# Optimization experiments

Hardware: AMD Instinct MI355X
Metric: run time of the kernel (lower is better)

Reference implementation:

```python
import jax, jax.numpy as jnp
import numpy as np

NUM_NODES = 100000
EMB = 16
LAT = 8
EDGE_DIM = 32
E = 1600000


def setup_inputs() -> dict:
    key = jax.random.key(0)
    ks = jax.random.split(key, 12)
    s = 0.05
    return {
        "edge_index": jax.random.randint(ks[0], (2, E), 0, NUM_NODES),
        "edge_attr": jax.random.normal(ks[1], (E, EDGE_DIM), dtype=jnp.float32),
        "node_emb": jax.random.normal(ks[2], (NUM_NODES, EMB), dtype=jnp.float32) * s,
        "ew_W1": jax.random.normal(ks[3], (EDGE_DIM, 64), dtype=jnp.float32) * s,
        "ew_b1": jnp.zeros((64,), jnp.float32),
        "ew_W2": jax.random.normal(ks[4], (64, EMB * LAT), dtype=jnp.float32) * s,
        "ew_b2": jnp.zeros((EMB * LAT,), jnp.float32),
        "root_W": jax.random.normal(ks[5], (EMB, LAT), dtype=jnp.float32) * s,
        "conv_b": jnp.zeros((LAT,), jnp.float32),
        "dec_W1": jax.random.normal(ks[6], (2 * LAT, 64), dtype=jnp.float32) * s,
        "dec_b1": jnp.zeros((64,), jnp.float32),
        "dec_W2": jax.random.normal(ks[7], (64, EDGE_DIM), dtype=jnp.float32) * s,
        "dec_b2": jnp.zeros((EDGE_DIM,), jnp.float32),
    }


def reference(edge_index, edge_attr, node_emb, ew_W1, ew_b1, ew_W2, ew_b2,
              root_W, conv_b, dec_W1, dec_b1, dec_W2, dec_b2):
    src, tgt = edge_index[0], edge_index[1]
    # edge MLP -> per-edge weight matrix (E, EMB, LAT)
    h = jax.nn.relu(edge_attr @ ew_W1 + ew_b1)
    theta = (h @ ew_W2 + ew_b2).reshape(-1, EMB, LAT)
    # per-edge matmul on gathered source features
    msg = jnp.einsum('ei,eio->eo', node_emb[src], theta)  # (E, LAT)
    # scatter-mean to targets
    agg = jax.ops.segment_sum(msg, tgt, num_segments=NUM_NODES)
    cnt = jax.ops.segment_sum(jnp.ones((msg.shape[0],), msg.dtype), tgt, num_segments=NUM_NODES)
    agg = agg / jnp.maximum(cnt, 1.0)[:, None]
    # NNConv root weight + bias
    latent = node_emb @ root_W + agg + conv_b  # (N, LAT)
    # decode: gather-concat-MLP on edges
    edge_in = jnp.concatenate([latent[src], latent[tgt]], axis=1)  # (E, 2*LAT)
    out = jax.nn.relu(edge_in @ dec_W1 + dec_b1) @ dec_W2 + dec_b2  # (E, EDGE_DIM)
    return out
```

## Files before the change

### kernel.cpp

```cpp
#include <hip/hip_runtime.h>
#include <hip/hip_bf16.h>

typedef __attribute__((ext_vector_type(8))) short  s16x8;
typedef __attribute__((ext_vector_type(4))) float  f32x4;

constexpr int EMB  = 16;
constexpr int LAT  = 8;
constexpr int EDIM = 32;
constexpr int HID  = 64;

constexpr int BSHIFT = 7;
constexpr int BNODES = 1 << BSHIFT;
constexpr int PCHUNK = 8192;

__device__ __forceinline__ short f2b(float f) {
  __hip_bfloat16 h = __float2bfloat16(f);
  return __builtin_bit_cast(short, h);
}
__device__ __forceinline__ float asf(unsigned int u) { return __builtin_bit_cast(float, u); }
__device__ __forceinline__ unsigned int pk2(float lo, float hi) {
  return ((unsigned int)(unsigned short)f2b(hi) << 16) |
         (unsigned int)(unsigned short)f2b(lo);
}

#define FIXSCALE 1.0995116277760e12f
#define FIXINV   9.094947017729282e-13

__global__ void prep_kernel(const float* __restrict__ W1, const float* __restrict__ W2,
                            const float* __restrict__ b2,
                            const float* __restrict__ dW1, const float* __restrict__ dW2,
                            short* __restrict__ W1c, short* __restrict__ W2p,
                            unsigned int* __restrict__ b2pp,
                            short* __restrict__ dW1c, short* __restrict__ dW2p) {
  int t = blockIdx.x * blockDim.x + threadIdx.x;
  if (t < 64 * 32) { int c = t / 32, k = t % 32; W1c[t] = f2b(W1[k * 64 + c]); }
  if (t < 8192) {
    int ct2 = t >> 10, kt = (t >> 9) & 1, lh = (t >> 7) & 3, r = (t >> 3) & 15, j = t & 7;
    int k = (kt * 2 + (j >> 2)) * 16 + lh * 4 + (j & 3);
    int i = 2 * ct2 + ((r >> 1) & 1);
    int o = 2 * (r >> 2) + (r & 1);
    W2p[t] = f2b(W2[k * 128 + i * 8 + o]);
  }
  if (t < 64) {
    int lh = t >> 4, slot = t & 15;
    int ct2 = slot >> 1, ih = slot & 1;
    int i = 2 * ct2 + ih;
    unsigned int lo = (unsigned short)f2b(b2[i * 8 + 2 * lh]);
    unsigned int hi = (unsigned short)f2b(b2[i * 8 + 2 * lh + 1]);
    b2pp[t] = (hi << 16) | lo;
  }
  if (t < 64 * 16) { int c = t / 16, k = t % 16; dW1c[t] = f2b(dW1[k * 64 + c]); }
  if (t < 2048) {
    int ct2 = t >> 10, kt = (t >> 9) & 1, lh = (t >> 7) & 3, r = (t >> 3) & 15, j = t & 7;
    int k = (kt * 2 + (j >> 2)) * 16 + lh * 4 + (j & 3);
    dW2p[t] = f2b(dW2[k * 32 + ct2 * 16 + r]);
  }
}

__global__ __launch_bounds__(256) void bhist_kernel(const int* __restrict__ ei,
                                                    int* __restrict__ bins,
                                                    int E, int nbuck) {
  __shared__ int h[1024];
  for (int i = threadIdx.x; i < nbuck; i += 256) h[i] = 0;
  __syncthreads();
  for (int e = blockIdx.x * blockDim.x + threadIdx.x; e < E; e += gridDim.x * blockDim.x)
    atomicAdd(&h[ei[E + e] >> BSHIFT], 1);
  __syncthreads();
  for (int i = threadIdx.x; i < nbuck; i += 256)
    if (h[i]) atomicAdd(&bins[i], h[i]);
}

__global__ __launch_bounds__(1024) void bscan_kernel(const int* __restrict__ bins,
                                                     int* __restrict__ bases,
                                                     int* __restrict__ cursor, int nbuck) {
  __shared__ int sh[1024];
  int tid = threadIdx.x;
  int v = (tid < nbuck) ? bins[tid] : 0;
  sh[tid] = v;
  __syncthreads();
  for (int off = 1; off < 1024; off <<= 1) {
    int t = (tid >= off) ? sh[tid - off] : 0;
    __syncthreads();
    sh[tid] += t;
    __syncthreads();
  }
  int ex = sh[tid] - v;
  if (tid < nbuck) { bases[tid] = ex; cursor[tid] = ex; }
  if (tid == 0) bases[nbuck] = sh[1023];
}

__global__ __launch_bounds__(256) void part_kernel(const int* __restrict__ ei,
                                                   int* __restrict__ cursor,
                                                   unsigned int* __restrict__ recs,
                                                   int E, int nbuck) {
  __shared__ int h[1024];
  __shared__ int gcl[1024];
  __shared__ int lr[1024];
  const int tid  = threadIdx.x;
  const int base = blockIdx.x * PCHUNK;

  for (int i = tid; i < nbuck; i += 256) { h[i] = 0; lr[i] = 0; }
  __syncthreads();
  for (int i = tid; i < PCHUNK; i += 256) {
    int e = base + i;
    if (e < E) atomicAdd(&h[ei[E + e] >> BSHIFT], 1);
  }
  __syncthreads();
  for (int i = tid; i < nbuck; i += 256)
    gcl[i] = h[i] ? atomicAdd(&cursor[i], h[i]) : 0;
  __syncthreads();
  for (int i = tid; i < PCHUNK; i += 256) {
    int e = base + i;
    if (e >= E) continue;
    int tgt = ei[E + e];
    int b = tgt >> BSHIFT;
    int p = gcl[b] + atomicAdd(&lr[b], 1);
    recs[p] = ((unsigned int)e << BSHIFT) | (unsigned int)(tgt & (BNODES - 1));
  }
}

__global__ __launch_bounds__(256, 3) void enc_mfma_kernel(
    const int* __restrict__ ei, const float* __restrict__ attr,
    const float* __restrict__ emb,
    const short* __restrict__ W1c, const float* __restrict__ b1,
    const short* __restrict__ W2p, const unsigned int* __restrict__ b2pp,
    short* __restrict__ ms, int E) {
  __shared__ short lds_w1[2048];
  __shared__ short lds_w2[8192];
  __shared__ float lds_b1[64];
  __shared__ unsigned int lds_b2[64];

  const int tid = threadIdx.x;
  const int w = tid >> 6, l = tid & 63;
  const int lh = l >> 4, ll = l & 15;
  const int ebase = blockIdx.x * 256 + w * 64;

  {
    reinterpret_cast<int4*>(lds_w1)[tid] = reinterpret_cast<const int4*>(W1c)[tid];
#pragma unroll
    for (int i = 0; i < 4; i++)
      reinterpret_cast<int4*>(lds_w2)[i * 256 + tid] =
          reinterpret_cast<const int4*>(W2p)[i * 256 + tid];
    if (tid < 64) lds_b1[tid] = b1[tid];
    if (tid < 64) lds_b2[tid] = b2pp[tid];
  }

  unsigned int xqp[8];
  {
    int ec = min(ebase + l, E - 1);
    int src = ei[ec];
    const float4* er = reinterpret_cast<const float4*>(emb) + (size_t)src * 4;
    float4 v0 = er[0], v1 = er[1], v2 = er[2], v3 = er[3];
    xqp[0] = pk2(v0.x, v0.y); xqp[1] = pk2(v0.z, v0.w);
    xqp[2] = pk2(v1.x, v1.y); xqp[3] = pk2(v1.z, v1.w);
    xqp[4] = pk2(v2.x, v2.y); xqp[5] = pk2(v2.z, v2.w);
    xqp[6] = pk2(v3.x, v3.y); xqp[7] = pk2(v3.z, v3.w);
  }

  s16x8 afs[4];
#pragma unroll
  for (int mt = 0; mt < 4; mt++) {
    int rowA = min(ebase + mt * 16 + ll, E - 1);
    const float4* ap = reinterpret_cast<const float4*>(attr + (size_t)rowA * EDIM + lh * 8);
    float4 a0 = ap[0], a1 = ap[1];
    afs[mt][0]=f2b(a0.x); afs[mt][1]=f2b(a0.y); afs[mt][2]=f2b(a0.z); afs[mt][3]=f2b(a0.w);
    afs[mt][4]=f2b(a1.x); afs[mt][5]=f2b(a1.y); afs[mt][6]=f2b(a1.z); afs[mt][7]=f2b(a1.w);
  }

  __syncthreads();

  const f32x4 z = {0.f, 0.f, 0.f, 0.f};

#pragma unroll
  for (int mt = 0; mt < 4; mt++) {
    f32x4 c1t[4];
#pragma unroll
    for (int ct = 0; ct < 4; ct++) {
      s16x8 b1f = *reinterpret_cast<const s16x8*>(lds_w1 + (ct * 16 + ll) * 32 + lh * 8);
      c1t[ct] = __builtin_amdgcn_mfma_f32_16x16x32_bf16(b1f, afs[mt], z, 0, 0, 0);
    }

    short hb[4][4];
#pragma unroll
    for (int ct = 0; ct < 4; ct++) {
      float4 bv = *reinterpret_cast<const float4*>(lds_b1 + ct * 16 + lh * 4);
      hb[ct][0] = f2b(fmaxf(c1t[ct][0] + bv.x, 0.f));
      hb[ct][1] = f2b(fmaxf(c1t[ct][1] + bv.y, 0.f));
      hb[ct][2] = f2b(fmaxf(c1t[ct][2] + bv.z, 0.f));
      hb[ct][3] = f2b(fmaxf(c1t[ct][3] + bv.w, 0.f));
    }
    s16x8 a2f0, a2f1;
#pragma unroll
    for (int j = 0; j < 8; j++) a2f0[j] = hb[(j >> 2)][j & 3];
#pragma unroll
    for (int j = 0; j < 8; j++) a2f1[j] = hb[2 + (j >> 2)][j & 3];

    const int srcl = mt * 16 + ll;
    unsigned int xs[8];
#pragma unroll
    for (int c = 0; c < 8; c++)
      xs[c] = (unsigned int)__shfl((int)xqp[c], srcl, 64);

    float q0 = 0.f, q1 = 0.f;
#pragma unroll
    for (int ct2 = 0; ct2 < 8; ct2++) {
      s16x8 f0 = *reinterpret_cast<const s16x8*>(lds_w2 + ((ct2 * 2 + 0) * 4 + lh) * 128 + ll * 8);
      s16x8 f1 = *reinterpret_cast<const s16x8*>(lds_w2 + ((ct2 * 2 + 1) * 4 + lh) * 128 + ll * 8);
      f32x4 c2 = __builtin_amdgcn_mfma_f32_16x16x32_bf16(f0, a2f0, z, 0, 0, 0);
      c2 = __builtin_amdgcn_mfma_f32_16x16x32_bf16(f1, a2f1, c2, 0, 0, 0);
      uint2 pp = *reinterpret_cast<const uint2*>(lds_b2 + lh * 16 + 2 * ct2);
      float b00 = asf(pp.x << 16), b01 = asf(pp.x & 0xffff0000u);
      float b10 = asf(pp.y << 16), b11 = asf(pp.y & 0xffff0000u);
      float xv0 = asf(xs[ct2] << 16);
      float xv1 = asf(xs[ct2] & 0xffff0000u);
      q0 = fmaf(xv0, c2[0] + b00, q0);
      q1 = fmaf(xv0, c2[1] + b01, q1);
      q0 = fmaf(xv1, c2[2] + b10, q0);
      q1 = fmaf(xv1, c2[3] + b11, q1);
    }
    int e = ebase + mt * 16 + ll;
    if (e < E)
      *reinterpret_cast<unsigned int*>(ms + (size_t)e * LAT + 2 * lh) = pk2(q0, q1);
  }
}

__global__ __launch_bounds__(256) void agg_kernel(
    const float* __restrict__ emb, const short* __restrict__ ms,
    const unsigned int* __restrict__ recs, const int* __restrict__ bases,
    const float* __restrict__ rootW, const float* __restrict__ convb,
    float* __restrict__ latent, int N) {
  __shared__ long long acc[BNODES][LAT];
  __shared__ int cnt[BNODES];
  __shared__ float rw[EMB * LAT];
  __shared__ float cb[LAT];

  const int tid = threadIdx.x;
  const int b = blockIdx.x;

  long long* af = &acc[0][0];
  for (int i = tid; i < BNODES * LAT; i += 256) af[i] = 0;
  if (tid < BNODES) cnt[tid] = 0;
  if (tid < EMB * LAT) rw[tid] = rootW[tid];
  if (tid < LAT) cb[tid] = convb[tid];
  __syncthreads();

  const int s = bases[b], epos = bases[b + 1];
  const uint4* mp = reinterpret_cast<const uint4*>(ms);
  for (int i = s + tid; i < epos; i += 256) {
    unsigned int r = recs[i];
    int eid = (int)(r >> BSHIFT);
    int tl  = (int)(r & (BNODES - 1));
    uint4 m = mp[(size_t)eid];
    float f0 = asf(m.x << 16), f1 = asf(m.x & 0xffff0000u);
    float f2 = asf(m.y << 16), f3 = asf(m.y & 0xffff0000u);
    float f4 = asf(m.z << 16), f5 = asf(m.z & 0xffff0000u);
    float f6 = asf(m.w << 16), f7 = asf(m.w & 0xffff0000u);
    atomicAdd((unsigned long long*)&acc[tl][0], (unsigned long long)(long long)(f0 * FIXSCALE));
    atomicAdd((unsigned long long*)&acc[tl][1], (unsigned long long)(long long)(f1 * FIXSCALE));
    atomicAdd((unsigned long long*)&acc[tl][2], (unsigned long long)(long long)(f2 * FIXSCALE));
    atomicAdd((unsigned long long*)&acc[tl][3], (unsigned long long)(long long)(f3 * FIXSCALE));
    atomicAdd((unsigned long long*)&acc[tl][4], (unsigned long long)(long long)(f4 * FIXSCALE));
    atomicAdd((unsigned long long*)&acc[tl][5], (unsigned long long)(long long)(f5 * FIXSCALE));
    atomicAdd((unsigned long long*)&acc[tl][6], (unsigned long long)(long long)(f6 * FIXSCALE));
    atomicAdd((unsigned long long*)&acc[tl][7], (unsigned long long)(long long)(f7 * FIXSCALE));
    atomicAdd(&cnt[tl], 1);
  }
  __syncthreads();

  int n = b * BNODES + tid;
  if (tid < BNODES && n < N) {
    float inv = 1.f / fmaxf((float)cnt[tid], 1.f);
    float r[LAT];
#pragma unroll
    for (int o = 0; o < LAT; o++)
      r[o] = fmaf((float)((double)acc[tid][o] * FIXINV), inv, cb[o]);

    float x[EMB];
    const float4* np4 = reinterpret_cast<const float4*>(emb) + (size_t)n * (EMB / 4);
#pragma unroll
    for (int i = 0; i < EMB / 4; i++) {
      float4 v = np4[i];
      x[4 * i + 0] = v.x; x[4 * i + 1] = v.y; x[4 * i + 2] = v.z; x[4 * i + 3] = v.w;
    }
#pragma unroll
    for (int i = 0; i < EMB; i++)
#pragma unroll
      for (int o = 0; o < LAT; o++) r[o] = fmaf(x[i], rw[i * LAT + o], r[o]);

    float4* lp = reinterpret_cast<float4*>(latent) + (size_t)n * 2;
    lp[0] = make_float4(r[0], r[1], r[2], r[3]);
    lp[1] = make_float4(r[4], r[5], r[6], r[7]);
  }
}

__global__ __launch_bounds__(256, 4) void dec_mfma_kernel(
    const int* __restrict__ ei, const float* __restrict__ lat,
    const short* __restrict__ dW1c, const float* __restrict__ db1,
    const short* __restrict__ dW2p, const float* __restrict__ db2,
    float* __restrict__ out, int E) {
  __shared__ short lds_w1[2048];
  __shared__ short lds_w2[2048];
  __shared__ float lds_b1[64];
  __shared__ float lds_b2[32];

  const int tid = threadIdx.x;
  const int w = tid >> 6, l = tid & 63;
  const int lh = l >> 4, ll = l & 15;
  const int ebase = blockIdx.x * 256 + w * 64;

  {
    if (tid < 128) {
      int4 v = reinterpret_cast<const int4*>(dW1c)[tid];
      int hid = tid >> 1, kb = (tid & 1) * 8;
      *reinterpret_cast<int4*>(lds_w1 + hid * 32 + kb) = v;
      *reinterpret_cast<int4*>(lds_w1 + hid * 32 + 16 + kb) = make_int4(0, 0, 0, 0);
    }
    reinterpret_cast<int4*>(lds_w2)[tid] = reinterpret_cast<const int4*>(dW2p)[tid];
    if (tid < 64) lds_b1[tid] = db1[tid];
    if (tid < 32) lds_b2[tid] = db2[tid];
  }
  __syncthreads();

  const f32x4 z = {0.f, 0.f, 0.f, 0.f};

#pragma unroll
  for (int mt = 0; mt < 4; mt++) {
    s16x8 af = (s16x8){0, 0, 0, 0, 0, 0, 0, 0};
    if (lh < 2) {
      int rowA = min(ebase + mt * 16 + ll, E - 1);
      int node = ei[(lh == 0 ? 0 : E) + rowA];
      const float4* lp = reinterpret_cast<const float4*>(lat + (size_t)node * LAT);
      float4 p0 = lp[0], p1 = lp[1];
      af[0]=f2b(p0.x); af[1]=f2b(p0.y); af[2]=f2b(p0.z); af[3]=f2b(p0.w);
      af[4]=f2b(p1.x); af[5]=f2b(p1.y); af[6]=f2b(p1.z); af[7]=f2b(p1.w);
    }

    f32x4 c1t[4];
#pragma unroll
    for (int ct = 0; ct < 4; ct++) {
      s16x8 b1f = *reinterpret_cast<const s16x8*>(lds_w1 + (ct * 16 + ll) * 32 + lh * 8);
      c1t[ct] = __builtin_amdgcn_mfma_f32_16x16x32_bf16(b1f, af, z, 0, 0, 0);
    }

    short hb[4][4];
#pragma unroll
    for (int ct = 0; ct < 4; ct++) {
      float4 bv = *reinterpret_cast<const float4*>(lds_b1 + ct * 16 + lh * 4);
      hb[ct][0] = f2b(fmaxf(c1t[ct][0] + bv.x, 0.f));
      hb[ct][1] = f2b(fmaxf(c1t[ct][1] + bv.y, 0.f));
      hb[ct][2] = f2b(fmaxf(c1t[ct][2] + bv.z, 0.f));
      hb[ct][3] = f2b(fmaxf(c1t[ct][3] + bv.w, 0.f));
    }
    s16x8 a2f0, a2f1;
#pragma unroll
    for (int j = 0; j < 8; j++) a2f0[j] = hb[(j >> 2)][j & 3];
#pragma unroll
    for (int j = 0; j < 8; j++) a2f1[j] = hb[2 + (j >> 2)][j & 3];

    int e = ebase + mt * 16 + ll;
#pragma unroll
    for (int ct2 = 0; ct2 < 2; ct2++) {
      s16x8 f0 = *reinterpret_cast<const s16x8*>(lds_w2 + ((ct2 * 2 + 0) * 4 + lh) * 128 + ll * 8);
      s16x8 f1 = *reinterpret_cast<const s16x8*>(lds_w2 + ((ct2 * 2 + 1) * 4 + lh) * 128 + ll * 8);
      f32x4 c2 = __builtin_amdgcn_mfma_f32_16x16x32_bf16(f0, a2f0, z, 0, 0, 0);
      c2 = __builtin_amdgcn_mfma_f32_16x16x32_bf16(f1, a2f1, c2, 0, 0, 0);
      float4 bv = *reinterpret_cast<const float4*>(lds_b2 + ct2 * 16 + lh * 4);
      if (e < E)
        *reinterpret_cast<float4*>(out + (size_t)e * EDIM + ct2 * 16 + lh * 4) =
            make_float4(c2[0] + bv.x, c2[1] + bv.y, c2[2] + bv.z, c2[3] + bv.w);
    }
  }
}

extern "C" void kernel_launch(void* const* d_in, const int* in_sizes, int n_in,
                              void* d_out, int out_size, void* d_ws, size_t ws_size,
                              hipStream_t stream) {
  const int*   ei    = (const int*)  d_in[0];
  const float* attr  = (const float*)d_in[1];
  const float* emb   = (const float*)d_in[2];
  const float* ewW1  = (const float*)d_in[3];
  const float* ewb1  = (const float*)d_in[4];
  const float* ewW2  = (const float*)d_in[5];
  const float* ewb2  = (const float*)d_in[6];
  const float* rootW = (const float*)d_in[7];
  const float* convb = (const float*)d_in[8];
  const float* dW1   = (const float*)d_in[9];
  const float* db1   = (const float*)d_in[10];
  const float* dW2   = (const float*)d_in[11];
  const float* db2   = (const float*)d_in[12];
  float* out = (float*)d_out;

  const int E     = in_sizes[0] / 2;
  const int N     = in_sizes[2] / EMB;
  const int nbuck = (N + BNODES - 1) >> BSHIFT;

  short* W1c  = (short*)d_ws;
  short* W2p  = W1c + 64 * 32;
  short* dW1c = W2p + 8192;
  short* dW2p = dW1c + 64 * 16;
  unsigned int* b2pp = (unsigned int*)(dW2p + 2048);
  short* ms   = (short*)(b2pp + 64);
  float* lat  = (float*)(ms + (size_t)E * LAT);
  unsigned int* recs = (unsigned int*)(lat + (size_t)N * LAT);
  int* bins   = (int*)(recs + E);
  int* bases  = bins + nbuck;
  int* cursor = bases + nbuck + 1;

  const int blocks_e = (E + 255) / 256;
  const int blocks_p = (E + PCHUNK - 1) / PCHUNK;

  hipMemsetAsync(bins, 0, (size_t)nbuck * sizeof(int), stream);
  prep_kernel<<<32, 256, 0, stream>>>(ewW1, ewW2, ewb2, dW1, dW2,
                                      W1c, W2p, b2pp, dW1c, dW2p);
  bhist_kernel<<<256, 256, 0, stream>>>(ei, bins, E, nbuck);
  bscan_kernel<<<1, 1024, 0, stream>>>(bins, bases, cursor, nbuck);
  part_kernel<<<blocks_p, 256, 0, stream>>>(ei, cursor, recs, E, nbuck);
  enc_mfma_kernel<<<blocks_e, 256, 0, stream>>>(ei, attr, emb, W1c, ewb1, W2p, b2pp,
                                                ms, E);
  agg_kernel<<<nbuck, 256, 0, stream>>>(emb, ms, recs, bases, rootW, convb, lat, N);
  dec_mfma_kernel<<<blocks_e, 256, 0, stream>>>(ei, lat, dW1c, db1, dW2p, db2, out, E);
}
```

Baseline: 220.7 us.

## Fuse edge encoder into bucketed aggregation kernel, dropping per-edge message buffer

Merges the per-edge MLP/message kernel into the target-bucket aggregation kernel. Each block walks its bucket's sorted edge records, computes messages with MFMA and accumulates them straight into LDS fixed-point accumulators, so the intermediate message array is never written to or read back from global memory. In exchange, edge_attr and source embeddings are now read in target-sorted, scattered order rather than coalesced, occupancy drops from three to two blocks per CU, and per-block work follows the uneven bucket sizes with only 782 blocks.

```diff
diff --git a/kernel.cpp b/kernel.cpp
--- a/kernel.cpp
+++ b/kernel.cpp
@@ -119,21 +119,27 @@
   }
 }
 
-__global__ __launch_bounds__(256, 3) void enc_mfma_kernel(
+__global__ __launch_bounds__(256, 2) void encagg_kernel(
     const int* __restrict__ ei, const float* __restrict__ attr,
     const float* __restrict__ emb,
     const short* __restrict__ W1c, const float* __restrict__ b1,
     const short* __restrict__ W2p, const unsigned int* __restrict__ b2pp,
-    short* __restrict__ ms, int E) {
+    const unsigned int* __restrict__ recs, const int* __restrict__ bases,
+    const float* __restrict__ rootW, const float* __restrict__ convb,
+    float* __restrict__ latent, int N, int E) {
   __shared__ short lds_w1[2048];
   __shared__ short lds_w2[8192];
   __shared__ float lds_b1[64];
   __shared__ unsigned int lds_b2[64];
+  __shared__ long long acc[BNODES][LAT];
+  __shared__ int cnt[BNODES];
+  __shared__ float rw[EMB * LAT];
+  __shared__ float cb[LAT];
 
   const int tid = threadIdx.x;
   const int w = tid >> 6, l = tid & 63;
   const int lh = l >> 4, ll = l & 15;
-  const int ebase = blockIdx.x * 256 + w * 64;
+  const int b = blockIdx.x;
 
   {
     reinterpret_cast<int4*>(lds_w1)[tid] = reinterpret_cast<const int4*>(W1c)[tid];
@@ -143,127 +149,99 @@
           reinterpret_cast<const int4*>(W2p)[i * 256 + tid];
     if (tid < 64) lds_b1[tid] = b1[tid];
     if (tid < 64) lds_b2[tid] = b2pp[tid];
-  }
-
-  unsigned int xqp[8];
-  {
-    int ec = min(ebase + l, E - 1);
-    int src = ei[ec];
-    const float4* er = reinterpret_cast<const float4*>(emb) + (size_t)src * 4;
-    float4 v0 = er[0], v1 = er[1], v2 = er[2], v3 = er[3];
-    xqp[0] = pk2(v0.x, v0.y); xqp[1] = pk2(v0.z, v0.w);
-    xqp[2] = pk2(v1.x, v1.y); xqp[3] = pk2(v1.z, v1.w);
-    xqp[4] = pk2(v2.x, v2.y); xqp[5] = pk2(v2.z, v2.w);
-    xqp[6] = pk2(v3.x, v3.y); xqp[7] = pk2(v3.z, v3.w);
-  }
-
-  s16x8 afs[4];
-#pragma unroll
-  for (int mt = 0; mt < 4; mt++) {
-    int rowA = min(ebase + mt * 16 + ll, E - 1);
-    const float4* ap = reinterpret_cast<const float4*>(attr + (size_t)rowA * EDIM + lh * 8);
-    float4 a0 = ap[0], a1 = ap[1];
-    afs[mt][0]=f2b(a0.x); afs[mt][1]=f2b(a0.y); afs[mt][2]=f2b(a0.z); afs[mt][3]=f2b(a0.w);
-    afs[mt][4]=f2b(a1.x); afs[mt][5]=f2b(a1.y); afs[mt][6]=f2b(a1.z); afs[mt][7]=f2b(a1.w);
-  }
-
-  __syncthreads();
-
+    long long* af0 = &acc[0][0];
+    for (int i = tid; i < BNODES * LAT; i += 256) af0[i] = 0;
+    if (tid < BNODES) cnt[tid] = 0;
+    if (tid < EMB * LAT) rw[tid] = rootW[tid];
+    if (tid < LAT) cb[tid] = convb[tid];
+  }
+  __syncthreads();
+
+  const int s = bases[b], epos = bases[b + 1];
+  const int nrec = epos - s;
   const f32x4 z = {0.f, 0.f, 0.f, 0.f};
 
-#pragma unroll
-  for (int mt = 0; mt < 4; mt++) {
-    f32x4 c1t[4];
-#pragma unroll
-    for (int ct = 0; ct < 4; ct++) {
-      s16x8 b1f = *reinterpret_cast<const s16x8*>(lds_w1 + (ct * 16 + ll) * 32 + lh * 8);
-      c1t[ct] = __builtin_amdgcn_mfma_f32_16x16x32_bf16(b1f, afs[mt], z, 0, 0, 0);
-    }
-
-    short hb[4][4];
-#pragma unroll
-    for (int ct = 0; ct < 4; ct++) {
-      float4 bv = *reinterpret_cast<const float4*>(lds_b1 + ct * 16 + lh * 4);
-      hb[ct][0] = f2b(fmaxf(c1t[ct][0] + bv.x, 0.f));
-      hb[ct][1] = f2b(fmaxf(c1t[ct][1] + bv.y, 0.f));
-      hb[ct][2] = f2b(fmaxf(c1t[ct][2] + bv.z, 0.f));
-      hb[ct][3] = f2b(fmaxf(c1t[ct][3] + bv.w, 0.f));
-    }
-    s16x8 a2f0, a2f1;
-#pragma unroll
-    for (int j = 0; j < 8; j++) a2f0[j] = hb[(j >> 2)][j & 3];
-#pragma unroll
-    for (int j = 0; j < 8; j++) a2f1[j] = hb[2 + (j >> 2)][j & 3];
-
-    const int srcl = mt * 16 + ll;
-    unsigned int xs[8];
-#pragma unroll
-    for (int c = 0; c < 8; c++)
-      xs[c] = (unsigned int)__shfl((int)xqp[c], srcl, 64);
-
-    float q0 = 0.f, q1 = 0.f;
-#pragma unroll
-    for (int ct2 = 0; ct2 < 8; ct2++) {
-      s16x8 f0 = *reinterpret_cast<const s16x8*>(lds_w2 + ((ct2 * 2 + 0) * 4 + lh) * 128 + ll * 8);
-      s16x8 f1 = *reinterpret_cast<const s16x8*>(lds_w2 + ((ct2 * 2 + 1) * 4 + lh) * 128 + ll * 8);
-      f32x4 c2 = __builtin_amdgcn_mfma_f32_16x16x32_bf16(f0, a2f0, z, 0, 0, 0);
-      c2 = __builtin_amdgcn_mfma_f32_16x16x32_bf16(f1, a2f1, c2, 0, 0, 0);
-      uint2 pp = *reinterpret_cast<const uint2*>(lds_b2 + lh * 16 + 2 * ct2);
-      float b00 = asf(pp.x << 16), b01 = asf(pp.x & 0xffff0000u);
-      float b10 = asf(pp.y << 16), b11 = asf(pp.y & 0xffff0000u);
-      float xv0 = asf(xs[ct2] << 16);
-      float xv1 = asf(xs[ct2] & 0xffff0000u);
-      q0 = fmaf(xv0, c2[0] + b00, q0);
-      q1 = fmaf(xv0, c2[1] + b01, q1);
-      q0 = fmaf(xv1, c2[2] + b10, q0);
-      q1 = fmaf(xv1, c2[3] + b11, q1);
-    }
-    int e = ebase + mt * 16 + ll;
-    if (e < E)
-      *reinterpret_cast<unsigned int*>(ms + (size_t)e * LAT + 2 * lh) = pk2(q0, q1);
-  }
-}
-
-__global__ __launch_bounds__(256) void agg_kernel(
-    const float* __restrict__ emb, const short* __restrict__ ms,
-    const unsigned int* __restrict__ recs, const int* __restrict__ bases,
-    const float* __restrict__ rootW, const float* __restrict__ convb,
-    float* __restrict__ latent, int N) {
-  __shared__ long long acc[BNODES][LAT];
-  __shared__ int cnt[BNODES];
-  __shared__ float rw[EMB * LAT];
-  __shared__ float cb[LAT];
-
-  const int tid = threadIdx.x;
-  const int b = blockIdx.x;
-
-  long long* af = &acc[0][0];
-  for (int i = tid; i < BNODES * LAT; i += 256) af[i] = 0;
-  if (tid < BNODES) cnt[tid] = 0;
-  if (tid < EMB * LAT) rw[tid] = rootW[tid];
-  if (tid < LAT) cb[tid] = convb[tid];
-  __syncthreads();
-
-  const int s = bases[b], epos = bases[b + 1];
-  const uint4* mp = reinterpret_cast<const uint4*>(ms);
-  for (int i = s + tid; i < epos; i += 256) {
-    unsigned int r = recs[i];
-    int eid = (int)(r >> BSHIFT);
-    int tl  = (int)(r & (BNODES - 1));
-    uint4 m = mp[(size_t)eid];
-    float f0 = asf(m.x << 16), f1 = asf(m.x & 0xffff0000u);
-    float f2 = asf(m.y << 16), f3 = asf(m.y & 0xffff0000u);
-    float f4 = asf(m.z << 16), f5 = asf(m.z & 0xffff0000u);
-    float f6 = asf(m.w << 16), f7 = asf(m.w & 0xffff0000u);
-    atomicAdd((unsigned long long*)&acc[tl][0], (unsigned long long)(long long)(f0 * FIXSCALE));
-    atomicAdd((unsigned long long*)&acc[tl][1], (unsigned long long)(long long)(f1 * FIXSCALE));
-    atomicAdd((unsigned long long*)&acc[tl][2], (unsigned long long)(long long)(f2 * FIXSCALE));
-    atomicAdd((unsigned long long*)&acc[tl][3], (unsigned long long)(long long)(f3 * FIXSCALE));
-    atomicAdd((unsigned long long*)&acc[tl][4], (unsigned long long)(long long)(f4 * FIXSCALE));
-    atomicAdd((unsigned long long*)&acc[tl][5], (unsigned long long)(long long)(f5 * FIXSCALE));
-    atomicAdd((unsigned long long*)&acc[tl][6], (unsigned long long)(long long)(f6 * FIXSCALE));
-    atomicAdd((unsigned long long*)&acc[tl][7], (unsigned long long)(long long)(f7 * FIXSCALE));
-    atomicAdd(&cnt[tl], 1);
+  for (int g = w * 64; g < nrec; g += 256) {
+    const int base = s + g;
+    int ridx = min(base + l, epos - 1);
+    unsigned int rec = recs[ridx];
+    int eid = (int)(rec >> BSHIFT);
+    int tl  = (int)(rec & (BNODES - 1));
+    unsigned int xqp[8];
+    {
+      int src = ei[eid];
+      const float4* er = reinterpret_cast<const float4*>(emb) + (size_t)src * 4;
+      float4 v0 = er[0], v1 = er[1], v2 = er[2], v3 = er[3];
+      xqp[0] = pk2(v0.x, v0.y); xqp[1] = pk2(v0.z, v0.w);
+      xqp[2] = pk2(v1.x, v1.y); xqp[3] = pk2(v1.z, v1.w);
+      xqp[4] = pk2(v2.x, v2.y); xqp[5] = pk2(v2.z, v2.w);
+      xqp[6] = pk2(v3.x, v3.y); xqp[7] = pk2(v3.z, v3.w);
+    }
+    s16x8 afs[4];
+#pragma unroll
+    for (int mt = 0; mt < 4; mt++) {
+      int rowE = __shfl(eid, mt * 16 + ll, 64);
+      const float4* ap = reinterpret_cast<const float4*>(attr + (size_t)rowE * EDIM + lh * 8);
+      float4 a0 = ap[0], a1 = ap[1];
+      afs[mt][0]=f2b(a0.x); afs[mt][1]=f2b(a0.y); afs[mt][2]=f2b(a0.z); afs[mt][3]=f2b(a0.w);
+      afs[mt][4]=f2b(a1.x); afs[mt][5]=f2b(a1.y); afs[mt][6]=f2b(a1.z); afs[mt][7]=f2b(a1.w);
+    }
+
+#pragma unroll
+    for (int mt = 0; mt < 4; mt++) {
+      f32x4 c1t[4];
+#pragma unroll
+      for (int ct = 0; ct < 4; ct++) {
+        s16x8 b1f = *reinterpret_cast<const s16x8*>(lds_w1 + (ct * 16 + ll) * 32 + lh * 8);
+        c1t[ct] = __builtin_amdgcn_mfma_f32_16x16x32_bf16(b1f, afs[mt], z, 0, 0, 0);
+      }
+      short hb[4][4];
+#pragma unroll
+      for (int ct = 0; ct < 4; ct++) {
+        float4 bv = *reinterpret_cast<const float4*>(lds_b1 + ct * 16 + lh * 4);
+        hb[ct][0] = f2b(fmaxf(c1t[ct][0] + bv.x, 0.f));
+        hb[ct][1] = f2b(fmaxf(c1t[ct][1] + bv.y, 0.f));
+        hb[ct][2] = f2b(fmaxf(c1t[ct][2] + bv.z, 0.f));
+        hb[ct][3] = f2b(fmaxf(c1t[ct][3] + bv.w, 0.f));
+      }
+      s16x8 a2f0, a2f1;
+#pragma unroll
+      for (int j = 0; j < 8; j++) a2f0[j] = hb[(j >> 2)][j & 3];
+#pragma unroll
+      for (int j = 0; j < 8; j++) a2f1[j] = hb[2 + (j >> 2)][j & 3];
+
+      const int srcl = mt * 16 + ll;
+      unsigned int xs[8];
+#pragma unroll
+      for (int c = 0; c < 8; c++)
+        xs[c] = (unsigned int)__shfl((int)xqp[c], srcl, 64);
+      int tlv = __shfl(tl, srcl, 64);
+
+      float q0 = 0.f, q1 = 0.f;
+#pragma unroll
+      for (int ct2 = 0; ct2 < 8; ct2++) {
+        s16x8 f0 = *reinterpret_cast<const s16x8*>(lds_w2 + ((ct2 * 2 + 0) * 4 + lh) * 128 + ll * 8);
+        s16x8 f1 = *reinterpret_cast<const s16x8*>(lds_w2 + ((ct2 * 2 + 1) * 4 + lh) * 128 + ll * 8);
+        f32x4 c2 = __builtin_amdgcn_mfma_f32_16x16x32_bf16(f0, a2f0, z, 0, 0, 0);
+        c2 = __builtin_amdgcn_mfma_f32_16x16x32_bf16(f1, a2f1, c2, 0, 0, 0);
+        uint2 pp = *reinterpret_cast<const uint2*>(lds_b2 + lh * 16 + 2 * ct2);
+        float b00 = asf(pp.x << 16), b01 = asf(pp.x & 0xffff0000u);
+        float b10 = asf(pp.y << 16), b11 = asf(pp.y & 0xffff0000u);
+        float xv0 = asf(xs[ct2] << 16);
+        float xv1 = asf(xs[ct2] & 0xffff0000u);
+        q0 = fmaf(xv0, c2[0] + b00, q0);
+        q1 = fmaf(xv0, c2[1] + b01, q1);
+        q0 = fmaf(xv1, c2[2] + b10, q0);
+        q1 = fmaf(xv1, c2[3] + b11, q1);
+      }
+      if (base + srcl < epos) {
+        atomicAdd((unsigned long long*)&acc[tlv][2 * lh],
+                  (unsigned long long)(long long)(q0 * FIXSCALE));
+        atomicAdd((unsigned long long*)&acc[tlv][2 * lh + 1],
+                  (unsigned long long)(long long)(q1 * FIXSCALE));
+        if (lh == 0) atomicAdd(&cnt[tlv], 1);
+      }
+    }
   }
   __syncthreads();
 
@@ -399,8 +377,7 @@
   short* dW1c = W2p + 8192;
   short* dW2p = dW1c + 64 * 16;
   unsigned int* b2pp = (unsigned int*)(dW2p + 2048);
-  short* ms   = (short*)(b2pp + 64);
-  float* lat  = (float*)(ms + (size_t)E * LAT);
+  float* lat  = (float*)(b2pp + 64);
   unsigned int* recs = (unsigned int*)(lat + (size_t)N * LAT);
   int* bins   = (int*)(recs + E);
   int* bases  = bins + nbuck;
@@ -415,8 +392,7 @@
   bhist_kernel<<<256, 256, 0, stream>>>(ei, bins, E, nbuck);
   bscan_kernel<<<1, 1024, 0, stream>>>(bins, bases, cursor, nbuck);
   part_kernel<<<blocks_p, 256, 0, stream>>>(ei, cursor, recs, E, nbuck);
-  enc_mfma_kernel<<<blocks_e, 256, 0, stream>>>(ei, attr, emb, W1c, ewb1, W2p, b2pp,
-                                                ms, E);
-  agg_kernel<<<nbuck, 256, 0, stream>>>(emb, ms, recs, bases, rootW, convb, lat, N);
+  encagg_kernel<<<nbuck, 256, 0, stream>>>(ei, attr, emb, W1c, ewb1, W2p, b2pp,
+                                           recs, bases, rootW, convb, lat, N, E);
   dec_mfma_kernel<<<blocks_e, 256, 0, stream>>>(ei, lat, dW1c, db1, dW2p, db2, out, E);
 }
```

Measured after the change: 223.2 us. Within noise of the previous version (+1.1%).
